# Kernel optimization log

Hardware: AMD Instinct MI355X
Metric: run time of the kernel (lower is better)

Reference implementation:

```python
import jax, jax.numpy as jnp
import numpy as np

T = 64        # time steps (batch)
N_SIDE = 256  # grid side, N = N_SIDE**2 flattened grid points
HID = 32      # hidden width of the shared per-point MLP
IN_CH = 5     # 5-point periodic stencil (l, l2, center, r, r2)


def _stencil_gather(x, n):
    """Replicates MLPConv._preprocess / make_px / get_value exactly.

    x: [T, n*n] flattened periodic grid. Returns [T, n*n, 5].
    get_value wraps indices via the piecewise rule (v-n if v>=n) and relies on
    numpy negative flat indexing for v=-1, which is the final `% (n*n)` here.
    Output position i_loop*n + j_loop reads grid flat index (j_loop+ik) + n*(i_loop+jk).
    """
    ii = jnp.arange(n)[:, None]  # i_loop (outer loop in make_px)
    jj = jnp.arange(n)[None, :]  # j_loop (inner loop)

    def idx(ik, jk):
        a = jj + ik
        a = jnp.where(a >= n, a - n, a)
        b = ii + jk
        b = jnp.where(b >= n, b - n, b)
        return ((a + n * b) % (n * n)).reshape(-1)  # [n*n]

    # channel order from _preprocess: cat([l, l2, px, r, r2], -1)
    offsets = [(-1, 0), (0, -1), (0, 0), (1, 0), (0, 1)]
    cols = jnp.stack([idx(ik, jk) for ik, jk in offsets], axis=-1)  # [n*n, 5]
    return x[:, cols]  # [T, n*n, 5]


def setup_inputs() -> dict:
    key = jax.random.key(0)
    ks = jax.random.split(key, 7)
    n2 = N_SIDE * N_SIDE
    x = jax.random.normal(ks[0], (T, n2), dtype=jnp.float32)
    # torch Linear weights are [out, in]; we store transposed [in, out] for x @ W.
    # Original init: xavier_normal * 10, bias zeros; scaled normals are equivalent for a baseline.
    def w(k, fan_in, fan_out):
        std = 10.0 * np.sqrt(2.0 / (fan_in + fan_out))
        return std * jax.random.normal(k, (fan_in, fan_out), dtype=jnp.float32)
    return {
        "x": x,
        "W0": w(ks[1], IN_CH, HID), "b0": jnp.zeros((HID,), jnp.float32),
        "W1": w(ks[2], HID, HID),   "b1": jnp.zeros((HID,), jnp.float32),
        "W2": w(ks[3], HID, 1),     "b2": jnp.zeros((1,), jnp.float32),
    }


def reference(x, W0, b0, W1, b1, W2, b2):
    # Note: the x_copy dual path in the torch forward never affects the returned
    # tensor (dead code), so the faithful math is a plain 3-layer MLP over the
    # 5-point periodic stencil gather, ELU between layers, no final activation.
    n = int(np.sqrt(x.shape[1]))
    px = _stencil_gather(x, n)                 # [T, N, 5]
    h = jax.nn.elu(px @ W0 + b0)               # [T, N, HID]
    h = jax.nn.elu(h @ W1 + b1)                # [T, N, HID]
    out = h @ W2 + b2                          # [T, N, 1]
    return out.squeeze(-1)                     # [T, N] (matches res.squeeze())
```

## Files before the change

### kernel.cpp

```cpp
#include <hip/hip_runtime.h>
#include <hip/hip_bf16.h>

#define T_STEPS 64
#define NS 256
#define N2 (NS * NS)
#define HID 32

typedef _Float16 half8 __attribute__((ext_vector_type(8)));
typedef float float4v __attribute__((ext_vector_type(4)));

#define TILES_TOTAL (T_STEPS * (N2 / 16))
#define TPW 16
#define WAVES_PER_BLOCK 4
#define NBLOCKS (TILES_TOTAL / (TPW * WAVES_PER_BLOCK))

__device__ __forceinline__ float elu(float z) {
    return (z > 0.0f) ? z : (__expf(z) - 1.0f);
}

__global__ __launch_bounds__(256) void mlpconv_mfma_kernel(
    const float* __restrict__ x,
    const float* __restrict__ W0, const float* __restrict__ b0,
    const float* __restrict__ W1, const float* __restrict__ b1,
    const float* __restrict__ W2, const float* __restrict__ b2,
    float* __restrict__ out)
{
    const int lane = threadIdx.x & 63;
    const int wid  = threadIdx.x >> 6;
    const int m    = lane & 15;
    const int kg   = lane >> 4;

    float w0c[5][8];
    #pragma unroll
    for (int c = 0; c < 5; ++c)
        #pragma unroll
        for (int i = 0; i < 8; ++i)
            w0c[c][i] = W0[c * HID + kg * 8 + i];
    float b0v[8];
    #pragma unroll
    for (int i = 0; i < 8; ++i) b0v[i] = b0[kg * 8 + i];

    half8 a0, a1;
    #pragma unroll
    for (int i = 0; i < 8; ++i) {
        a0[i] = (_Float16)W1[(kg * 8 + i) * HID + m];
        a1[i] = (_Float16)W1[(kg * 8 + i) * HID + 16 + m];
    }
    float4v c0i, c1i;
    #pragma unroll
    for (int r = 0; r < 4; ++r) {
        c0i[r] = b1[kg * 4 + r];
        c1i[r] = b1[16 + kg * 4 + r];
    }
    float w2a[4], w2b[4];
    #pragma unroll
    for (int r = 0; r < 4; ++r) {
        w2a[r] = W2[kg * 4 + r];
        w2b[r] = W2[16 + kg * 4 + r];
    }
    const float b2v = b2[0];

    const int gw = blockIdx.x * WAVES_PER_BLOCK + wid;
    const int g0 = gw * TPW;

    for (int l = 0; l < TPW; ++l) {
        const int g  = g0 + l;
        const int t  = g >> 12;
        const int s0 = (g & 4095) << 4;
        const int s  = s0 + m;
        const float* xt = x + ((size_t)t << 16);

        const int sl  = (s - 1)  & (N2 - 1);
        const int sl2 = (s - NS) & (N2 - 1);
        const int sr  = (s & ~(NS - 1)) | ((s + 1) & (NS - 1));
        const int sr2 = (s + NS) & (N2 - 1);

        const float in0 = xt[sl];
        const float in1 = xt[sl2];
        const float in2 = xt[s];
        const float in3 = xt[sr];
        const float in4 = xt[sr2];

        half8 hfrag;
        #pragma unroll
        for (int i = 0; i < 8; ++i) {
            float z = b0v[i];
            z = fmaf(in0, w0c[0][i], z);
            z = fmaf(in1, w0c[1][i], z);
            z = fmaf(in2, w0c[2][i], z);
            z = fmaf(in3, w0c[3][i], z);
            z = fmaf(in4, w0c[4][i], z);
            hfrag[i] = (_Float16)elu(z);
        }

        float4v d0 = __builtin_amdgcn_mfma_f32_16x16x32_f16(a0, hfrag, c0i, 0, 0, 0);
        float4v d1 = __builtin_amdgcn_mfma_f32_16x16x32_f16(a1, hfrag, c1i, 0, 0, 0);

        float part = 0.0f;
        #pragma unroll
        for (int r = 0; r < 4; ++r) {
            part = fmaf(elu(d0[r]), w2a[r], part);
            part = fmaf(elu(d1[r]), w2b[r], part);
        }
        part += __shfl_xor(part, 16, 64);
        part += __shfl_xor(part, 32, 64);

        if (kg == 0) {
            out[((size_t)t << 16) + s] = part + b2v;
        }
    }
}

extern "C" void kernel_launch(void* const* d_in, const int* in_sizes, int n_in,
                              void* d_out, int out_size, void* d_ws, size_t ws_size,
                              hipStream_t stream) {
    const float* x  = (const float*)d_in[0];
    const float* W0 = (const float*)d_in[1];
    const float* b0 = (const float*)d_in[2];
    const float* W1 = (const float*)d_in[3];
    const float* b1 = (const float*)d_in[4];
    const float* W2 = (const float*)d_in[5];
    const float* b2 = (const float*)d_in[6];
    float* out = (float*)d_out;

    mlpconv_mfma_kernel<<<dim3(NBLOCKS), dim3(256), 0, stream>>>(
        x, W0, b0, W1, b1, W2, b2, out);
}
```

Before: 149.8 us.

## Use packed fp16 math for first layer and specialize interior row addressing

Computes the first-layer stencil matvec and its ELU in packed half2 arithmetic (pk_fma, exp2-based ELU) instead of scalar fp32, halving VALU instruction count for that stage. Each wave's 16 tiles now map to one row, so interior rows use simple offset addressing with a single wrap fix, while edge rows keep the modular index path. The tile loop is fully unrolled and launch bounds add an occupancy hint. This trades precision in the first layer (fp16 accumulation of 5 products and fp16 exp) for fewer ALU ops.

```diff
diff --git a/kernel.cpp b/kernel.cpp
--- a/kernel.cpp
+++ b/kernel.cpp
@@ -1,24 +1,97 @@
 #include <hip/hip_runtime.h>
 #include <hip/hip_bf16.h>
+#include <hip/hip_fp16.h>
 
 #define T_STEPS 64
 #define NS 256
 #define N2 (NS * NS)
 #define HID 32
 
+typedef _Float16 h2    __attribute__((ext_vector_type(2)));
 typedef _Float16 half8 __attribute__((ext_vector_type(8)));
-typedef float float4v __attribute__((ext_vector_type(4)));
+typedef float    float4v __attribute__((ext_vector_type(4)));
 
-#define TILES_TOTAL (T_STEPS * (N2 / 16))
 #define TPW 16
 #define WAVES_PER_BLOCK 4
+#define TILES_TOTAL (T_STEPS * (N2 / 16))
 #define NBLOCKS (TILES_TOTAL / (TPW * WAVES_PER_BLOCK))
 
-__device__ __forceinline__ float elu(float z) {
+__device__ __forceinline__ float eluf(float z) {
     return (z > 0.0f) ? z : (__expf(z) - 1.0f);
 }
 
-__global__ __launch_bounds__(256) void mlpconv_mfma_kernel(
+__device__ __forceinline__ h2 splat2(float f) {
+    _Float16 h = (_Float16)f;
+    h2 r; r[0] = h; r[1] = h;
+    return r;
+}
+
+__device__ __forceinline__ h2 elu2(h2 z) {
+    h2 zero; zero[0] = (_Float16)0.f; zero[1] = (_Float16)0.f;
+    h2 zm = __builtin_elementwise_min(z, zero);
+    h2 e  = __builtin_elementwise_exp2(zm * (_Float16)1.442695041f);
+    h2 em1 = e + (_Float16)(-1.0f);
+    return __builtin_elementwise_max(z, em1);
+}
+
+struct Frags {
+    h2 w0h[5][4];
+    h2 b0h[4];
+    half8 a0, a1;
+    float4v c0i, c1i;
+    float w2a[4], w2b[4];
+    float b2v;
+};
+
+__device__ __forceinline__ void tile_body(
+    const Frags& F, float in0, float in1, float in2, float in3, float in4,
+    int kg, float* __restrict__ outp)
+{
+    h2 zw[4];
+    #pragma unroll
+    for (int w = 0; w < 4; ++w) zw[w] = F.b0h[w];
+    {
+        h2 p;
+        p = splat2(in0);
+        #pragma unroll
+        for (int w = 0; w < 4; ++w) zw[w] = p * F.w0h[0][w] + zw[w];
+        p = splat2(in1);
+        #pragma unroll
+        for (int w = 0; w < 4; ++w) zw[w] = p * F.w0h[1][w] + zw[w];
+        p = splat2(in2);
+        #pragma unroll
+        for (int w = 0; w < 4; ++w) zw[w] = p * F.w0h[2][w] + zw[w];
+        p = splat2(in3);
+        #pragma unroll
+        for (int w = 0; w < 4; ++w) zw[w] = p * F.w0h[3][w] + zw[w];
+        p = splat2(in4);
+        #pragma unroll
+        for (int w = 0; w < 4; ++w) zw[w] = p * F.w0h[4][w] + zw[w];
+    }
+    half8 hf;
+    #pragma unroll
+    for (int w = 0; w < 4; ++w) {
+        h2 hw = elu2(zw[w]);
+        hf[2 * w]     = hw[0];
+        hf[2 * w + 1] = hw[1];
+    }
+
+    float4v d0 = __builtin_amdgcn_mfma_f32_16x16x32_f16(F.a0, hf, F.c0i, 0, 0, 0);
+    float4v d1 = __builtin_amdgcn_mfma_f32_16x16x32_f16(F.a1, hf, F.c1i, 0, 0, 0);
+
+    float part = 0.0f;
+    #pragma unroll
+    for (int r = 0; r < 4; ++r) {
+        part = fmaf(eluf(d0[r]), F.w2a[r], part);
+        part = fmaf(eluf(d1[r]), F.w2b[r], part);
+    }
+    part += __shfl_xor(part, 16, 64);
+    part += __shfl_xor(part, 32, 64);
+
+    if (kg == 0) *outp = part + F.b2v;
+}
+
+__global__ __launch_bounds__(256, 4) void mlpconv_pk_mfma_kernel(
     const float* __restrict__ x,
     const float* __restrict__ W0, const float* __restrict__ b0,
     const float* __restrict__ W1, const float* __restrict__ b1,
@@ -30,83 +103,62 @@
     const int m    = lane & 15;
     const int kg   = lane >> 4;
 
-    float w0c[5][8];
+    Frags F;
     #pragma unroll
     for (int c = 0; c < 5; ++c)
         #pragma unroll
-        for (int i = 0; i < 8; ++i)
-            w0c[c][i] = W0[c * HID + kg * 8 + i];
-    float b0v[8];
+        for (int w = 0; w < 4; ++w) {
+            F.w0h[c][w][0] = (_Float16)W0[c * HID + kg * 8 + 2 * w];
+            F.w0h[c][w][1] = (_Float16)W0[c * HID + kg * 8 + 2 * w + 1];
+        }
     #pragma unroll
-    for (int i = 0; i < 8; ++i) b0v[i] = b0[kg * 8 + i];
-
-    half8 a0, a1;
+    for (int w = 0; w < 4; ++w) {
+        F.b0h[w][0] = (_Float16)b0[kg * 8 + 2 * w];
+        F.b0h[w][1] = (_Float16)b0[kg * 8 + 2 * w + 1];
+    }
     #pragma unroll
     for (int i = 0; i < 8; ++i) {
-        a0[i] = (_Float16)W1[(kg * 8 + i) * HID + m];
-        a1[i] = (_Float16)W1[(kg * 8 + i) * HID + 16 + m];
+        F.a0[i] = (_Float16)W1[(kg * 8 + i) * HID + m];
+        F.a1[i] = (_Float16)W1[(kg * 8 + i) * HID + 16 + m];
     }
-    float4v c0i, c1i;
     #pragma unroll
     for (int r = 0; r < 4; ++r) {
-        c0i[r] = b1[kg * 4 + r];
-        c1i[r] = b1[16 + kg * 4 + r];
+        F.c0i[r] = b1[kg * 4 + r];
+        F.c1i[r] = b1[16 + kg * 4 + r];
+        F.w2a[r] = W2[kg * 4 + r];
+        F.w2b[r] = W2[16 + kg * 4 + r];
     }
-    float w2a[4], w2b[4];
-    #pragma unroll
-    for (int r = 0; r < 4; ++r) {
-        w2a[r] = W2[kg * 4 + r];
-        w2b[r] = W2[16 + kg * 4 + r];
-    }
-    const float b2v = b2[0];
+    F.b2v = b2[0];
 
-    const int gw = blockIdx.x * WAVES_PER_BLOCK + wid;
-    const int g0 = gw * TPW;
+    const int gw    = blockIdx.x * WAVES_PER_BLOCK + wid;
+    const int g0    = gw * TPW;
+    const int t     = g0 >> 12;
+    const int sbase = (g0 & 4095) << 4;
+    const int i0    = sbase >> 8;
 
-    for (int l = 0; l < TPW; ++l) {
-        const int g  = g0 + l;
-        const int t  = g >> 12;
-        const int s0 = (g & 4095) << 4;
-        const int s  = s0 + m;
-        const float* xt = x + ((size_t)t << 16);
+    const float* xt   = x   + ((size_t)t << 16);
+    float*       outt = out + ((size_t)t << 16);
 
-        const int sl  = (s - 1)  & (N2 - 1);
-        const int sl2 = (s - NS) & (N2 - 1);
-        const int sr  = (s & ~(NS - 1)) | ((s + 1) & (NS - 1));
-        const int sr2 = (s + NS) & (N2 - 1);
-
-        const float in0 = xt[sl];
-        const float in1 = xt[sl2];
-        const float in2 = xt[s];
-        const float in3 = xt[sr];
-        const float in4 = xt[sr2];
-
-        half8 hfrag;
+    if (i0 != 0 && i0 != 255) {
         #pragma unroll
-        for (int i = 0; i < 8; ++i) {
-            float z = b0v[i];
-            z = fmaf(in0, w0c[0][i], z);
-            z = fmaf(in1, w0c[1][i], z);
-            z = fmaf(in2, w0c[2][i], z);
-            z = fmaf(in3, w0c[3][i], z);
-            z = fmaf(in4, w0c[4][i], z);
-            hfrag[i] = (_Float16)elu(z);
+        for (int l = 0; l < TPW; ++l) {
+            const int s = sbase + 16 * l + m;
+            const float in0 = xt[s - 1];
+            const float in1 = xt[s - NS];
+            const float in2 = xt[s];
+            const float in3 = (l == 15 && m == 15) ? xt[s + 1 - NS] : xt[s + 1];
+            const float in4 = xt[s + NS];
+            tile_body(F, in0, in1, in2, in3, in4, kg, outt + s);
         }
-
-        float4v d0 = __builtin_amdgcn_mfma_f32_16x16x32_f16(a0, hfrag, c0i, 0, 0, 0);
-        float4v d1 = __builtin_amdgcn_mfma_f32_16x16x32_f16(a1, hfrag, c1i, 0, 0, 0);
-
-        float part = 0.0f;
+    } else {
         #pragma unroll
-        for (int r = 0; r < 4; ++r) {
-            part = fmaf(elu(d0[r]), w2a[r], part);
-            part = fmaf(elu(d1[r]), w2b[r], part);
-        }
-        part += __shfl_xor(part, 16, 64);
-        part += __shfl_xor(part, 32, 64);
-
-        if (kg == 0) {
-            out[((size_t)t << 16) + s] = part + b2v;
+        for (int l = 0; l < TPW; ++l) {
+            const int s   = sbase + 16 * l + m;
+            const int sl  = (s - 1)  & (N2 - 1);
+            const int sl2 = (s - NS) & (N2 - 1);
+            const int sr  = (s & ~(NS - 1)) | ((s + 1) & (NS - 1));
+            const int sr2 = (s + NS) & (N2 - 1);
+            tile_body(F, xt[sl], xt[sl2], xt[s], xt[sr], xt[sr2], kg, outt + s);
         }
     }
 }
@@ -123,6 +175,6 @@
     const float* b2 = (const float*)d_in[6];
     float* out = (float*)d_out;
 
-    mlpconv_mfma_kernel<<<dim3(NBLOCKS), dim3(256), 0, stream>>>(
+    mlpconv_pk_mfma_kernel<<<dim3(NBLOCKS), dim3(256), 0, stream>>>(
         x, W0, b0, W1, b1, W2, b2, out);
 }
```

Measured after the change: 137.6 us. 1.09x faster.
